# Kernel tuning notes

Hardware: AMD Instinct MI355X
Metric: run time of the kernel (lower is better)

The kernel has to match this reference:

```python
import jax, jax.numpy as jnp
import numpy as np

B, T, D, DE, S, P = 16384, 2, 1024, 512, 4, 4  # batch, tasks, inp_dim, expt_dim, share, specific


def setup_inputs() -> dict:
    key = jax.random.key(0)
    ks = jax.random.split(key, 8)
    sc = 0.02
    return {
        "x0": jax.random.normal(ks[0], (B, D), jnp.float32),
        "x1": jax.random.normal(ks[1], (B, D), jnp.float32),
        "W_share": jax.random.normal(ks[2], (S, D, DE), jnp.float32) * sc,
        "b_share": jnp.zeros((S, DE), jnp.float32),
        "W_spcf": jax.random.normal(ks[3], (T, P, D, DE), jnp.float32) * sc,
        "b_spcf": jnp.zeros((T, P, DE), jnp.float32),
        "W_gate": jax.random.normal(ks[4], (T, D, S + P), jnp.float32) * sc,
        "b_gate": jnp.zeros((T, S + P), jnp.float32),
    }


def reference(x0, x1, W_share, b_share, W_spcf, b_spcf, W_gate, b_gate):
    # cat_x: [B, T, D]
    x = jnp.stack([x0, x1], axis=1)
    # per-task gate over all S+P experts: [B, T, S+P]
    gates = jax.nn.softmax(jnp.einsum("btd,tde->bte", x, W_gate) + b_gate, axis=-1)
    # shared experts applied to every task's input: [B, T, S, DE]
    share = jax.nn.relu(jnp.einsum("btd,sdf->btsf", x, W_share) + b_share[None, None])
    # task-specific experts applied to their own task input: [B, T, P, DE]
    spcf = jax.nn.relu(jnp.einsum("btd,tpdf->btpf", x, W_spcf) + b_spcf[None])
    experts = jnp.concatenate([share, spcf], axis=2)  # [B, T, S+P, DE]
    # softmax-gated mixture: [B, T, DE] (== list of per-task [B, DE] in the original)
    return jnp.einsum("bte,btef->btf", gates, experts)
```

## Files before the change

### kernel.cpp

```cpp
#include <hip/hip_runtime.h>
#include <stdint.h>

#define kB  16384
#define kD  1024
#define kDE 512

typedef __bf16 bf16x8 __attribute__((ext_vector_type(8)));
typedef float  f32x4  __attribute__((ext_vector_type(4)));

__device__ __forceinline__ unsigned short f2bf(float f) {
    union { float f; unsigned u; } v; v.f = f;
    unsigned r = v.u + 0x7FFFu + ((v.u >> 16) & 1u);
    return (unsigned short)(r >> 16);
}

__device__ __forceinline__ void async16(unsigned short* lds, const unsigned short* g) {
    __builtin_amdgcn_global_load_lds(
        (const __attribute__((address_space(1))) unsigned int*)g,
        (__attribute__((address_space(3))) unsigned int*)lds, 16, 0, 0);
}

__global__ __launch_bounds__(256) void prep_w(const float* __restrict__ Wsh,
                                              const float* __restrict__ Wsp,
                                              unsigned short* __restrict__ Wt) {
    __shared__ float tile[32][33];
    const int slot = blockIdx.z;
    const int k0 = blockIdx.x * 32;
    const int n0 = blockIdx.y * 32;
    const float* src = (slot < 4) ? (Wsh + (size_t)slot * kD * kDE)
                                  : (Wsp + (size_t)(slot - 4) * kD * kDE);
    const int tx = threadIdx.x, ty = threadIdx.y;
#pragma unroll
    for (int i = 0; i < 4; i++)
        tile[ty + i * 8][tx] = src[(size_t)(k0 + ty + i * 8) * kDE + n0 + tx];
    __syncthreads();
    unsigned short* dst = Wt + (size_t)slot * kDE * kD;
#pragma unroll
    for (int i = 0; i < 4; i++)
        dst[(size_t)(n0 + ty + i * 8) * kD + k0 + tx] = f2bf(tile[tx][ty + i * 8]);
}

__global__ __launch_bounds__(256) void prep_b(const float* __restrict__ bsh,
                                              const float* __restrict__ bsp,
                                              float* __restrict__ bc) {
    int i = blockIdx.x * 256 + threadIdx.x;
    int n = i & 511, e = (i >> 9) & 7, t = i >> 12;
    bc[i] = (e < 4) ? bsh[e * 512 + n] : bsp[(t * 4 + (e - 4)) * 512 + n];
}

__global__ __launch_bounds__(256) void conv_gate(
    const float* __restrict__ x0, const float* __restrict__ x1,
    const float* __restrict__ Wg, const float* __restrict__ bg,
    unsigned short* __restrict__ xb, float* __restrict__ g) {
    const int wid = threadIdx.x >> 6, lane = threadIdx.x & 63;
    const int r = blockIdx.x * 4 + wid;
    const int t = r >> 14, b = r & 16383;
    const float* xrow = (t ? x1 : x0) + (size_t)b * kD;
    unsigned short* xbrow = xb + (size_t)(t * kB + b) * kD;
    const float* Wgt = Wg + t * kD * 8;
    float p[8] = {0.f,0.f,0.f,0.f,0.f,0.f,0.f,0.f};
#pragma unroll
    for (int it = 0; it < 4; it++) {
        const int d0 = it * 256 + lane * 4;
        const float4 v = *(const float4*)(xrow + d0);
        ushort4 h;
        h.x = f2bf(v.x); h.y = f2bf(v.y); h.z = f2bf(v.z); h.w = f2bf(v.w);
        *(ushort4*)(xbrow + d0) = h;
        const float xv[4] = {v.x, v.y, v.z, v.w};
#pragma unroll
        for (int j = 0; j < 4; j++) {
            const float* wrow = Wgt + (size_t)(d0 + j) * 8;
#pragma unroll
            for (int e = 0; e < 8; e++) p[e] += xv[j] * wrow[e];
        }
    }
#pragma unroll
    for (int e = 0; e < 8; e++) {
        float v = p[e];
#pragma unroll
        for (int s = 1; s < 64; s <<= 1) v += __shfl_xor(v, s, 64);
        p[e] = v;
    }
    float lg[8];
#pragma unroll
    for (int e = 0; e < 8; e++) lg[e] = p[e] + bg[t * 8 + e];
    float mx = lg[0];
#pragma unroll
    for (int e = 1; e < 8; e++) mx = fmaxf(mx, lg[e]);
    float s = 0.f;
#pragma unroll
    for (int e = 0; e < 8; e++) { lg[e] = __expf(lg[e] - mx); s += lg[e]; }
    const float inv = 1.f / s;
    if (lane == 0) {
        float* gp = g + (size_t)(t * kB + b) * 8;
        float4 g0 = {lg[0]*inv, lg[1]*inv, lg[2]*inv, lg[3]*inv};
        float4 g1 = {lg[4]*inv, lg[5]*inv, lg[6]*inv, lg[7]*inv};
        *(float4*)gp = g0;
        *(float4*)(gp + 4) = g1;
    }
}

__global__ __launch_bounds__(512, 2) void moe_gemm(
    const unsigned short* __restrict__ xb, const unsigned short* __restrict__ Wt,
    const float* __restrict__ g, const float* __restrict__ bc,
    float* __restrict__ out) {
    __shared__ __align__(16) unsigned short As[2][128 * 64];
    __shared__ __align__(16) unsigned short Bs[2][8 * 64 * 64];

    const int bid = blockIdx.x;
    const int swz = (bid & 7) * 256 + (bid >> 3);
    const int ct = swz & 7;
    const int rt = (swz >> 3) & 127;
    const int t  = swz >> 10;
    const int n0 = ct * 64;

    const int tid = threadIdx.x, wid = tid >> 6, lane = tid & 63;
    const int wr = wid >> 2, wc = wid & 3;

    const int swzChunk = ((lane & 7) ^ ((lane >> 3) & 7)) * 8;
    const unsigned short* aSrc = xb + (size_t)t * kB * kD +
        (size_t)(rt * 128 + wid * 16 + (lane >> 3)) * kD + swzChunk;
    const int slot = (wid < 4) ? wid : (4 + t * 4 + (wid - 4));
    const unsigned short* bSrc = Wt + (size_t)slot * kDE * kD +
        (size_t)(n0 + (lane >> 3)) * kD + swzChunk;

    const int rAbase = (wr * 64 + (lane & 15)) * 64;
    const int bOff   = (wc * 16 + (lane & 15)) * 64;
    const int lx     = lane & 7;
    const int kg     = lane >> 4;

    f32x4 acc[8][4];
#pragma unroll
    for (int e = 0; e < 8; e++)
#pragma unroll
        for (int m = 0; m < 4; m++) acc[e][m] = (f32x4){0.f, 0.f, 0.f, 0.f};

    bf16x8 af[4];
    bf16x8 bfr[4];

#define STAGE_A(buf, ktn)                                                      \
    _Pragma("unroll")                                                          \
    for (int i = 0; i < 2; i++)                                                \
        async16(&As[buf][wid * 1024 + i * 512], aSrc + (ktn) * 64 + i * 8 * kD);

#define STAGE_B(buf, ktn, j0, jn)                                              \
    _Pragma("unroll")                                                          \
    for (int j = (j0); j < (j0) + (jn); j++)                                   \
        async16(&Bs[buf][wid * 4096 + j * 512], bSrc + (ktn) * 64 + j * 8 * kD);

#define READ_A(buf, ks)                                                        \
    _Pragma("unroll")                                                          \
    for (int m = 0; m < 4; m++)                                                \
        af[m] = *(const bf16x8*)&As[buf][rAbase + m * 1024 +                   \
                                         ((((ks) * 4 + kg) ^ lx) << 3)];

#define READ_B(buf, ks, e0)                                                    \
    _Pragma("unroll")                                                          \
    for (int i = 0; i < 4; i++)                                                \
        bfr[i] = *(const bf16x8*)&Bs[buf][((e0) + i) * 4096 + bOff +           \
                                          ((((ks) * 4 + kg) ^ lx) << 3)];

#define MFMA_CLUSTER(e0)                                                       \
    asm volatile("s_waitcnt lgkmcnt(0)" ::: "memory");                         \
    __builtin_amdgcn_sched_barrier(0);                                         \
    __builtin_amdgcn_s_setprio(1);                                             \
    _Pragma("unroll")                                                          \
    for (int i = 0; i < 4; i++)                                                \
        _Pragma("unroll")                                                      \
        for (int m = 0; m < 4; m++)                                            \
            acc[(e0) + i][m] = __builtin_amdgcn_mfma_f32_16x16x32_bf16(        \
                af[m], bfr[i], acc[(e0) + i][m], 0, 0, 0);                     \
    __builtin_amdgcn_s_setprio(0);

#define STEP(cur, nxt, ktn)                                                    \
    {                                                                          \
                           \
        STAGE_A(nxt, ktn);                                                     \
        asm volatile("s_waitcnt vmcnt(2)" ::: "memory");                       \
        __builtin_amdgcn_s_barrier();                                          \
        __builtin_amdgcn_sched_barrier(0);                                     \
        READ_A(cur, 0);                                                        \
        READ_B(cur, 0, 0);                                                     \
        MFMA_CLUSTER(0);                                                       \
                                                     \
        READ_B(cur, 0, 4);                                                     \
        STAGE_B(nxt, ktn, 0, 3);                                               \
        __builtin_amdgcn_s_barrier();                                          \
        MFMA_CLUSTER(4);                                                       \
                                                     \
        READ_A(cur, 1);                                                        \
        READ_B(cur, 1, 0);                                                     \
        STAGE_B(nxt, ktn, 3, 3);                                               \
        __builtin_amdgcn_s_barrier();                                          \
        MFMA_CLUSTER(0);                                                       \
                                                     \
        READ_B(cur, 1, 4);                                                     \
        STAGE_B(nxt, ktn, 6, 2);                                               \
        __builtin_amdgcn_s_barrier();                                          \
        MFMA_CLUSTER(4);                                                       \
           \
        __builtin_amdgcn_s_barrier();                                          \
        __builtin_amdgcn_sched_barrier(0);                                     \
    }

    STAGE_A(0, 0);
    STAGE_B(0, 0, 0, 8);

    for (int kt2 = 0; kt2 < 8; ++kt2) {
        const int ka = kt2 * 2 + 1;
        const int kb = (kt2 * 2 + 2) & 15;
        STEP(0, 1, ka)
        STEP(1, 0, kb)
    }
    asm volatile("s_waitcnt vmcnt(0)" ::: "memory");

#undef STAGE_A
#undef STAGE_B
#undef READ_A
#undef READ_B
#undef MFMA_CLUSTER
#undef STEP

    const int col = n0 + wc * 16 + (lane & 15);
    float bv[8];
#pragma unroll
    for (int e = 0; e < 8; e++) bv[e] = bc[(t * 8 + e) * kDE + col];

#pragma unroll
    for (int m = 0; m < 4; m++) {
        const int r0 = rt * 128 + wr * 64 + m * 16 + kg * 4;
        f32x4 oq = (f32x4){0.f, 0.f, 0.f, 0.f};
#pragma unroll
        for (int q = 0; q < 4; q++) {
            const float* gp = g + ((size_t)t * kB + r0 + q) * 8;
            const float4 ga = *(const float4*)gp;
            const float4 gb = *(const float4*)(gp + 4);
            const float gv[8] = {ga.x, ga.y, ga.z, ga.w, gb.x, gb.y, gb.z, gb.w};
            float s = 0.f;
#pragma unroll
            for (int e = 0; e < 8; e++)
                s += gv[e] * fmaxf(acc[e][m][q] + bv[e], 0.f);
            oq[q] = s;
        }
#pragma unroll
        for (int q = 0; q < 4; q++)
            out[((size_t)(r0 + q) * 2 + t) * kDE + col] = oq[q];
    }
}

extern "C" void kernel_launch(void* const* d_in, const int* in_sizes, int n_in,
                              void* d_out, int out_size, void* d_ws, size_t ws_size,
                              hipStream_t stream) {
    const float* x0  = (const float*)d_in[0];
    const float* x1  = (const float*)d_in[1];
    const float* Wsh = (const float*)d_in[2];
    const float* bsh = (const float*)d_in[3];
    const float* Wsp = (const float*)d_in[4];
    const float* bsp = (const float*)d_in[5];
    const float* Wg  = (const float*)d_in[6];
    const float* bg  = (const float*)d_in[7];
    float* out = (float*)d_out;

    char* ws = (char*)d_ws;
    unsigned short* xb = (unsigned short*)ws;
    unsigned short* Wt = (unsigned short*)(ws + 67108864);
    float* g  = (float*)(ws + 67108864 + 12582912);
    float* bc = (float*)(ws + 67108864 + 12582912 + 1048576);

    prep_w<<<dim3(32, 16, 12), dim3(32, 8), 0, stream>>>(Wsh, Wsp, Wt);
    prep_b<<<dim3(32), dim3(256), 0, stream>>>(bsh, bsp, bc);
    conv_gate<<<dim3(8192), dim3(256), 0, stream>>>(x0, x1, Wg, bg, xb, g);
    moe_gemm<<<dim3(2048), dim3(512), 0, stream>>>(xb, Wt, g, bc, out);
}
```

Baseline: 450.4 us.

## Retile MoE GEMM to 256-row tiles with two expert groups per block

Each GEMM block now covers 256 rows and processes the 8 experts in two groups of 4. After each group it folds the result into a running gated output accumulator, replacing one 128-row block that held all 8 expert accumulators. This doubles A-tile reuse across the expert columns and halves the block count, aiming to cut redundant global and LDS traffic for B and A. In exchange the A tile is streamed twice per block and the pipeline gets more barriers. The gate projection loads are also vectorised to float4.

Result: slower. 472.6 us (+4.9%).

```diff
diff --git a/kernel.cpp b/kernel.cpp
--- a/kernel.cpp
+++ b/kernel.cpp
@@ -70,8 +70,12 @@
 #pragma unroll
         for (int j = 0; j < 4; j++) {
             const float* wrow = Wgt + (size_t)(d0 + j) * 8;
-#pragma unroll
-            for (int e = 0; e < 8; e++) p[e] += xv[j] * wrow[e];
+            const float4 wa = *(const float4*)wrow;
+            const float4 wb = *(const float4*)(wrow + 4);
+            p[0] += xv[j] * wa.x; p[1] += xv[j] * wa.y;
+            p[2] += xv[j] * wa.z; p[3] += xv[j] * wa.w;
+            p[4] += xv[j] * wb.x; p[5] += xv[j] * wb.y;
+            p[6] += xv[j] * wb.z; p[7] += xv[j] * wb.w;
         }
     }
 #pragma unroll
@@ -104,113 +108,141 @@
     const unsigned short* __restrict__ xb, const unsigned short* __restrict__ Wt,
     const float* __restrict__ g, const float* __restrict__ bc,
     float* __restrict__ out) {
-    __shared__ __align__(16) unsigned short As[2][128 * 64];
-    __shared__ __align__(16) unsigned short Bs[2][8 * 64 * 64];
+    __shared__ __align__(16) unsigned short As[2][256 * 64];
+    __shared__ __align__(16) unsigned short Bs[2][4 * 64 * 64];
 
     const int bid = blockIdx.x;
-    const int swz = (bid & 7) * 256 + (bid >> 3);
-    const int ct = swz & 7;
-    const int rt = (swz >> 3) & 127;
-    const int t  = swz >> 10;
-    const int n0 = ct * 64;
+    const int swz = (bid & 7) * 128 + (bid >> 3);
+    const int t   = swz >> 9;
+    const int rem = swz & 511;
+    const int rt  = rem >> 3;
+    const int ct  = rem & 7;
+    const int rowBase = rt * 256, n0 = ct * 64;
 
     const int tid = threadIdx.x, wid = tid >> 6, lane = tid & 63;
     const int wr = wid >> 2, wc = wid & 3;
+    const int lx = lane & 7, kg = lane >> 4;
 
     const int swzChunk = ((lane & 7) ^ ((lane >> 3) & 7)) * 8;
     const unsigned short* aSrc = xb + (size_t)t * kB * kD +
-        (size_t)(rt * 128 + wid * 16 + (lane >> 3)) * kD + swzChunk;
-    const int slot = (wid < 4) ? wid : (4 + t * 4 + (wid - 4));
-    const unsigned short* bSrc = Wt + (size_t)slot * kDE * kD +
-        (size_t)(n0 + (lane >> 3)) * kD + swzChunk;
-
-    const int rAbase = (wr * 64 + (lane & 15)) * 64;
-    const int bOff   = (wc * 16 + (lane & 15)) * 64;
-    const int lx     = lane & 7;
-    const int kg     = lane >> 4;
-
-    f32x4 acc[8][4];
-#pragma unroll
-    for (int e = 0; e < 8; e++)
-#pragma unroll
-        for (int m = 0; m < 4; m++) acc[e][m] = (f32x4){0.f, 0.f, 0.f, 0.f};
-
-    bf16x8 af[4];
-    bf16x8 bfr[4];
-
-#define STAGE_A(buf, ktn)                                                      \
-    _Pragma("unroll")                                                          \
-    for (int i = 0; i < 2; i++)                                                \
-        async16(&As[buf][wid * 1024 + i * 512], aSrc + (ktn) * 64 + i * 8 * kD);
-
-#define STAGE_B(buf, ktn, j0, jn)                                              \
-    _Pragma("unroll")                                                          \
-    for (int j = (j0); j < (j0) + (jn); j++)                                   \
-        async16(&Bs[buf][wid * 4096 + j * 512], bSrc + (ktn) * 64 + j * 8 * kD);
+        (size_t)(rowBase + wid * 8 + (lane >> 3)) * kD + swzChunk;
+    const size_t bSrcLane = (size_t)(n0 + wid * 8 + (lane >> 3)) * kD + swzChunk;
+
+    const int rAB = (wr * 128 + (lane & 15)) * 64;
+    const int rBB = (wc * 16 + (lane & 15)) * 64;
+
+    f32x4 acc[4][8];
+    f32x4 oacc[8];
+    bf16x8 af[8], b0, b1;
+#pragma unroll
+    for (int m = 0; m < 8; m++) oacc[m] = (f32x4){0.f, 0.f, 0.f, 0.f};
+
+#define STAGE_A(buf, ktn, rnd)                                                 \
+    async16(&As[buf][(rnd) * 4096 + wid * 512],                                \
+            aSrc + (size_t)(rnd) * 64 * kD + (ktn) * 64);
+
+#define STAGE_B(buf, ktn, gn, e)                                               \
+    async16(&Bs[buf][(e) * 4096 + wid * 512],                                  \
+            Wt + (size_t)(((gn) ? 4 + t * 4 : 0) + (e)) * (kDE * kD) +         \
+                bSrcLane + (ktn) * 64);
 
 #define READ_A(buf, ks)                                                        \
     _Pragma("unroll")                                                          \
-    for (int m = 0; m < 4; m++)                                                \
-        af[m] = *(const bf16x8*)&As[buf][rAbase + m * 1024 +                   \
+    for (int m = 0; m < 8; m++)                                                \
+        af[m] = *(const bf16x8*)&As[buf][rAB + m * 1024 +                      \
                                          ((((ks) * 4 + kg) ^ lx) << 3)];
 
-#define READ_B(buf, ks, e0)                                                    \
-    _Pragma("unroll")                                                          \
-    for (int i = 0; i < 4; i++)                                                \
-        bfr[i] = *(const bf16x8*)&Bs[buf][((e0) + i) * 4096 + bOff +           \
-                                          ((((ks) * 4 + kg) ^ lx) << 3)];
-
-#define MFMA_CLUSTER(e0)                                                       \
-    asm volatile("s_waitcnt lgkmcnt(0)" ::: "memory");                         \
-    __builtin_amdgcn_sched_barrier(0);                                         \
+#define READ_B(buf, ks, e, dst)                                                \
+    dst = *(const bf16x8*)&Bs[buf][(e) * 4096 + rBB +                          \
+                                   ((((ks) * 4 + kg) ^ lx) << 3)];
+
+#define CLUST(eA, eB)                                                          \
     __builtin_amdgcn_s_setprio(1);                                             \
     _Pragma("unroll")                                                          \
-    for (int i = 0; i < 4; i++)                                                \
-        _Pragma("unroll")                                                      \
-        for (int m = 0; m < 4; m++)                                            \
-            acc[(e0) + i][m] = __builtin_amdgcn_mfma_f32_16x16x32_bf16(        \
-                af[m], bfr[i], acc[(e0) + i][m], 0, 0, 0);                     \
+    for (int m = 0; m < 8; m++) {                                              \
+        acc[eA][m] = __builtin_amdgcn_mfma_f32_16x16x32_bf16(af[m], b0,        \
+                                                             acc[eA][m], 0, 0, 0); \
+        acc[eB][m] = __builtin_amdgcn_mfma_f32_16x16x32_bf16(af[m], b1,        \
+                                                             acc[eB][m], 0, 0, 0); \
+    }                                                                          \
     __builtin_amdgcn_s_setprio(0);
 
-#define STEP(cur, nxt, ktn)                                                    \
+#define WAIT_ENTER                                                             \
+    asm volatile("s_waitcnt lgkmcnt(0)" ::: "memory");                         \
+    __builtin_amdgcn_sched_barrier(0);
+
+#define TILE(cur, nxt, in)                                                     \
     {                                                                          \
-                           \
-        STAGE_A(nxt, ktn);                                                     \
-        asm volatile("s_waitcnt vmcnt(2)" ::: "memory");                       \
-        __builtin_amdgcn_s_barrier();                                          \
-        __builtin_amdgcn_sched_barrier(0);                                     \
+        const int ktn_ = (in) & 15;                                            \
+        const int gn_  = ((in) >> 4) & 1;                                      \
+                  \
         READ_A(cur, 0);                                                        \
-        READ_B(cur, 0, 0);                                                     \
-        MFMA_CLUSTER(0);                                                       \
-                                                     \
-        READ_B(cur, 0, 4);                                                     \
-        STAGE_B(nxt, ktn, 0, 3);                                               \
-        __builtin_amdgcn_s_barrier();                                          \
-        MFMA_CLUSTER(4);                                                       \
-                                                     \
+        READ_B(cur, 0, 0, b0); READ_B(cur, 0, 1, b1);                          \
+        STAGE_A(nxt, ktn_, 0); STAGE_A(nxt, ktn_, 1);                          \
+        STAGE_A(nxt, ktn_, 2); STAGE_A(nxt, ktn_, 3);                          \
+        __builtin_amdgcn_s_barrier();                                          \
+        WAIT_ENTER;                                                            \
+        CLUST(0, 1);                                                           \
+        __builtin_amdgcn_s_barrier();                                          \
+                                \
+        READ_B(cur, 0, 2, b0); READ_B(cur, 0, 3, b1);                          \
+        STAGE_B(nxt, ktn_, gn_, 0); STAGE_B(nxt, ktn_, gn_, 1);                \
+        __builtin_amdgcn_s_barrier();                                          \
+        WAIT_ENTER;                                                            \
+        CLUST(2, 3);                                                           \
+        __builtin_amdgcn_s_barrier();                                          \
+                                \
         READ_A(cur, 1);                                                        \
-        READ_B(cur, 1, 0);                                                     \
-        STAGE_B(nxt, ktn, 3, 3);                                               \
-        __builtin_amdgcn_s_barrier();                                          \
-        MFMA_CLUSTER(0);                                                       \
-                                                     \
-        READ_B(cur, 1, 4);                                                     \
-        STAGE_B(nxt, ktn, 6, 2);                                               \
-        __builtin_amdgcn_s_barrier();                                          \
-        MFMA_CLUSTER(4);                                                       \
-           \
-        __builtin_amdgcn_s_barrier();                                          \
-        __builtin_amdgcn_sched_barrier(0);                                     \
-    }
-
-    STAGE_A(0, 0);
-    STAGE_B(0, 0, 0, 8);
-
-    for (int kt2 = 0; kt2 < 8; ++kt2) {
-        const int ka = kt2 * 2 + 1;
-        const int kb = (kt2 * 2 + 2) & 15;
-        STEP(0, 1, ka)
-        STEP(1, 0, kb)
+        READ_B(cur, 1, 0, b0); READ_B(cur, 1, 1, b1);                          \
+        STAGE_B(nxt, ktn_, gn_, 2); STAGE_B(nxt, ktn_, gn_, 3);                \
+        __builtin_amdgcn_s_barrier();                                          \
+        WAIT_ENTER;                                                            \
+        CLUST(0, 1);                                                           \
+        __builtin_amdgcn_s_barrier();                                          \
+               \
+        READ_B(cur, 1, 2, b0); READ_B(cur, 1, 3, b1);                          \
+        asm volatile("s_waitcnt vmcnt(0)" ::: "memory");                       \
+        __builtin_amdgcn_s_barrier();                                          \
+        WAIT_ENTER;                                                            \
+        CLUST(2, 3);                                                           \
+        __builtin_amdgcn_s_barrier();                                          \
+    }
+
+    STAGE_A(0, 0, 0); STAGE_A(0, 0, 1); STAGE_A(0, 0, 2); STAGE_A(0, 0, 3);
+    STAGE_B(0, 0, 0, 0); STAGE_B(0, 0, 0, 1); STAGE_B(0, 0, 0, 2); STAGE_B(0, 0, 0, 3);
+    asm volatile("s_waitcnt vmcnt(0)" ::: "memory");
+    __builtin_amdgcn_s_barrier();
+
+    const int col = n0 + wc * 16 + (lane & 15);
+
+    for (int gi = 0; gi < 2; ++gi) {
+#pragma unroll
+        for (int e = 0; e < 4; e++)
+#pragma unroll
+            for (int m = 0; m < 8; m++) acc[e][m] = (f32x4){0.f, 0.f, 0.f, 0.f};
+
+        for (int kk = 0; kk < 8; ++kk) {
+            const int i = gi * 16 + kk * 2;
+            TILE(0, 1, i + 1)
+            TILE(1, 0, (i + 2) & 31)
+        }
+
+        float bv[4];
+#pragma unroll
+        for (int e = 0; e < 4; e++) bv[e] = bc[(t * 8 + gi * 4 + e) * kDE + col];
+        const float* gBase = g + (size_t)t * kB * 8 + gi * 4;
+#pragma unroll
+        for (int m = 0; m < 8; m++) {
+            const int r0 = rowBase + wr * 128 + m * 16 + kg * 4;
+#pragma unroll
+            for (int q = 0; q < 4; q++) {
+                const float4 gq = *(const float4*)(gBase + (size_t)(r0 + q) * 8);
+                oacc[m][q] += gq.x * fmaxf(acc[0][m][q] + bv[0], 0.f)
+                            + gq.y * fmaxf(acc[1][m][q] + bv[1], 0.f)
+                            + gq.z * fmaxf(acc[2][m][q] + bv[2], 0.f)
+                            + gq.w * fmaxf(acc[3][m][q] + bv[3], 0.f);
+            }
+        }
     }
     asm volatile("s_waitcnt vmcnt(0)" ::: "memory");
 
@@ -218,33 +250,16 @@
 #undef STAGE_B
 #undef READ_A
 #undef READ_B
-#undef MFMA_CLUSTER
-#undef STEP
-
-    const int col = n0 + wc * 16 + (lane & 15);
-    float bv[8];
-#pragma unroll
-    for (int e = 0; e < 8; e++) bv[e] = bc[(t * 8 + e) * kDE + col];
-
-#pragma unroll
-    for (int m = 0; m < 4; m++) {
-        const int r0 = rt * 128 + wr * 64 + m * 16 + kg * 4;
-        f32x4 oq = (f32x4){0.f, 0.f, 0.f, 0.f};
-#pragma unroll
-        for (int q = 0; q < 4; q++) {
-            const float* gp = g + ((size_t)t * kB + r0 + q) * 8;
-            const float4 ga = *(const float4*)gp;
-            const float4 gb = *(const float4*)(gp + 4);
-            const float gv[8] = {ga.x, ga.y, ga.z, ga.w, gb.x, gb.y, gb.z, gb.w};
-            float s = 0.f;
-#pragma unroll
-            for (int e = 0; e < 8; e++)
-                s += gv[e] * fmaxf(acc[e][m][q] + bv[e], 0.f);
-            oq[q] = s;
-        }
+#undef CLUST
+#undef WAIT_ENTER
+#undef TILE
+
+#pragma unroll
+    for (int m = 0; m < 8; m++) {
+        const int r0 = rowBase + wr * 128 + m * 16 + kg * 4;
 #pragma unroll
         for (int q = 0; q < 4; q++)
-            out[((size_t)(r0 + q) * 2 + t) * kDE + col] = oq[q];
+            out[((size_t)(r0 + q) * 2 + t) * kDE + col] = oacc[m][q];
     }
 }
 
@@ -270,5 +285,5 @@
     prep_w<<<dim3(32, 16, 12), dim3(32, 8), 0, stream>>>(Wsh, Wsp, Wt);
     prep_b<<<dim3(32), dim3(256), 0, stream>>>(bsh, bsp, bc);
     conv_gate<<<dim3(8192), dim3(256), 0, stream>>>(x0, x1, Wg, bg, xb, g);
-    moe_gemm<<<dim3(2048), dim3(512), 0, stream>>>(xb, Wt, g, bc, out);
-}
+    moe_gemm<<<dim3(1024), dim3(512), 0, stream>>>(xb, Wt, g, bc, out);
+}
```
